# Kernel optimization log

Hardware: AMD Instinct MI355X
Metric: run time of the kernel (lower is better)

The kernel has to match this reference:

```python
import jax, jax.numpy as jnp
import numpy as np

S, B, D, E2 = 2048, 32, 1024, 1024  # src_len, batch, dec_hid_dim, 2*enc_hid_dim


def setup_inputs() -> dict:
    key = jax.random.key(0)
    k1, k2, k3, k4, k5 = jax.random.split(key, 5)
    scale = 1.0 / np.sqrt(D)
    return {
        "dec_prev_hidden": jax.random.normal(k1, (B, D), dtype=jnp.float32),
        "enc_outputs": jax.random.normal(k2, (S, B, E2), dtype=jnp.float32),
        "Wb": jax.random.normal(k3, (D, D), dtype=jnp.float32) * scale,
        "Wc": jax.random.normal(k4, (D, E2), dtype=jnp.float32) * scale,
        "Wa": jax.random.normal(k5, (D,), dtype=jnp.float32) * scale,
    }


def reference(dec_prev_hidden, enc_outputs, Wb, Wc, Wa):
    # weighted_s_t_1: [B, D] broadcast over seq axis; weighted_H: [S, B, D]
    weighted_s = jnp.einsum('bd,ed->be', dec_prev_hidden, Wb)          # [B, D]
    weighted_H = jnp.einsum('sbe,de->sbd', enc_outputs, Wc)            # [S, B, D]
    score = jnp.einsum('sbd,d->sb', jnp.tanh(weighted_H + weighted_s), Wa)  # [S, B]
    # torch F.softmax with no dim on a 3-D tensor -> dim=0 (seq axis)
    attn = jax.nn.softmax(score, axis=0)                               # [S, B]
    # bmm([B,1,S], [B,S,2E]) -> [B,1,2E], then permute -> [1,B,2E]
    context = jnp.einsum('sb,sbe->be', attn, enc_outputs)              # [B, 2E]
    return context[None, :, :]                                         # [1, B, 2E]
```

## Files before the change

kernel.cpp:

```cpp
#include <hip/hip_runtime.h>
#include <hip/hip_bf16.h>
#include <stdint.h>

#define S_LEN 2048
#define BATCH 32
#define MROWS (S_LEN*BATCH)

typedef __attribute__((ext_vector_type(8))) short bf16x8;
typedef __attribute__((ext_vector_type(4))) float f32x4;
typedef unsigned short ushort_t;

__device__ inline unsigned int pk2bf(float a, float b) {
  float2 t; t.x = a; t.y = b;
  __hip_bfloat162 h = __float22bfloat162_rn(t);
  union { __hip_bfloat162 h; unsigned int u; } c; c.h = h;
  return c.u;
}

__device__ inline float bflo(unsigned int u) { return __uint_as_float(u << 16); }
__device__ inline float bfhi(unsigned int u) { return __uint_as_float(u & 0xffff0000u); }

__device__ inline void gload_lds16(const void* g, void* l) {
  __builtin_amdgcn_global_load_lds(
      (const __attribute__((address_space(1))) unsigned int*)g,
      (__attribute__((address_space(3))) unsigned int*)l, 16, 0, 0);
}

__device__ inline float fast_tanh(float x) {
  float e = __expf(2.0f * x);
  return 1.0f - 2.0f / (e + 1.0f);
}

__global__ __launch_bounds__(256) void prep_small_kernel(
    const float* __restrict__ dec, const float* __restrict__ Wb,
    const float* __restrict__ Wc, ushort_t* __restrict__ WcBf,
    float* __restrict__ wsum, float* __restrict__ outZero, int outN)
{
  const int t = threadIdx.x;
  const int bid = blockIdx.x;
  if (bid < 64) {
    const int base = bid * 16384;
    for (int i = 0; i < 16; ++i) {
      int idx = base + i * 1024 + t * 4;
      float4 v = *(const float4*)(Wc + idx);
      uint2 w; w.x = pk2bf(v.x, v.y); w.y = pk2bf(v.z, v.w);
      *(uint2*)(WcBf + idx) = w;
    }
  } else if (bid < 96) {
    const int j = bid - 64;
    __shared__ float sdec[32][65];
    __shared__ float swb[32][65];
    const int b = t & 31, nl = t >> 5;
    float acc0 = 0.f, acc1 = 0.f, acc2 = 0.f, acc3 = 0.f;
    for (int c = 0; c < 16; ++c) {
      __syncthreads();
      for (int idx = t; idx < 2048; idx += 256) {
        int rr = idx >> 6, dd = idx & 63;
        sdec[rr][dd] = dec[rr * 1024 + c * 64 + dd];
        swb[rr][dd]  = Wb[(size_t)(j * 32 + rr) * 1024 + c * 64 + dd];
      }
      __syncthreads();
      #pragma unroll 8
      for (int dd = 0; dd < 64; ++dd) {
        float dv = sdec[b][dd];
        acc0 += dv * swb[nl][dd];
        acc1 += dv * swb[nl + 8][dd];
        acc2 += dv * swb[nl + 16][dd];
        acc3 += dv * swb[nl + 24][dd];
      }
    }
    wsum[b * 1024 + j * 32 + nl]      = acc0;
    wsum[b * 1024 + j * 32 + nl + 8]  = acc1;
    wsum[b * 1024 + j * 32 + nl + 16] = acc2;
    wsum[b * 1024 + j * 32 + nl + 24] = acc3;
  } else {
    float4 z = make_float4(0.f, 0.f, 0.f, 0.f);
    const int n4 = outN >> 2;
    for (int i = t; i < n4; i += 256)
      ((float4*)outZero)[i] = z;
  }
}

__global__ __launch_bounds__(256, 4) void score_kernel(
    const float4* __restrict__ encF4, ushort_t* __restrict__ encBf,
    const ushort_t* __restrict__ WcBf, const float* __restrict__ wsum,
    const float* __restrict__ Wa, float* __restrict__ scoreP8T)
{
  __shared__ ushort_t Ab[128][64];
  __shared__ ushort_t Bb[128][64];
  __shared__ float scorep[128];

  const int tid = threadIdx.x;
  const int lane = tid & 63;
  const int l15 = lane & 15, q = lane >> 4;
  const int r7 = l15 & 7;
  const int wid = tid >> 6;
  const int wr = wid >> 1, wc = wid & 1;
  const int bid = blockIdx.x;
  const int mi = bid & 15, nblk = (bid >> 4) & 7, mg = bid >> 7;
  const size_t rowBase = (size_t)(mg * 16 + mi) * 128;

  if (tid < 128) scorep[tid] = 0.f;

  const int tRow = tid >> 4;
  const int f4 = tid & 15;
  const int swzT = (((f4 >> 1) ^ (tRow & 7)) * 8) + ((f4 & 1) * 4);

  int bOff[4], dOff[4];
  #pragma unroll
  for (int k = 0; k < 4; ++k) {
    const int s = k * 256 + tid;
    const int r = s >> 3, c = s & 7;
    bOff[k] = (int)((nblk * 128 + r) * 1024 + ((c ^ (r & 7)) * 8));
    dOff[k] = s * 8;
  }
  ushort_t* const aL = &Ab[0][0];
  ushort_t* const bL = &Bb[0][0];

  int aRow[4], bRow[4];
  #pragma unroll
  for (int m = 0; m < 4; ++m) aRow[m] = (wr * 64 + m * 16 + l15) * 64;
  #pragma unroll
  for (int n = 0; n < 4; ++n) bRow[n] = (wc * 64 + n * 16 + l15) * 64;
  const int ch0 = (q ^ r7) * 8;
  const int ch1 = ((4 + q) ^ r7) * 8;

  f32x4 acc[4][4];
  #pragma unroll
  for (int m = 0; m < 4; ++m)
    #pragma unroll
    for (int n = 0; n < 4; ++n) { f32x4 z = {0.f,0.f,0.f,0.f}; acc[m][n] = z; }

  for (int kt = 0; kt < 16; ++kt) {
    const int ko = kt * 64;
    #pragma unroll
    for (int k = 0; k < 4; ++k)
      gload_lds16(WcBf + ko + bOff[k], bL + dOff[k]);

    float4 av[8];
    #pragma unroll
    for (int k = 0; k < 8; ++k)
      av[k] = encF4[(rowBase + k * 16 + tRow) * 256 + kt * 16 + f4];

    #pragma unroll
    for (int k = 0; k < 8; ++k) {
      uint2 w;
      w.x = pk2bf(av[k].x, av[k].y);
      w.y = pk2bf(av[k].z, av[k].w);
      const int r = k * 16 + tRow;
      *(uint2*)(aL + r * 64 + swzT) = w;
      if (nblk == 0)
        *(uint2*)(encBf + (rowBase + r) * 1024 + ko + f4 * 4) = w;
    }
    __syncthreads();

    #pragma unroll
    for (int kk = 0; kk < 2; ++kk) {
      const int cho = kk ? ch1 : ch0;
      bf16x8 af[4], bv[4];
      #pragma unroll
      for (int m = 0; m < 4; ++m) af[m] = *(const bf16x8*)(aL + aRow[m] + cho);
      #pragma unroll
      for (int n = 0; n < 4; ++n) bv[n] = *(const bf16x8*)(bL + bRow[n] + cho);
      #pragma unroll
      for (int m = 0; m < 4; ++m)
        #pragma unroll
        for (int n = 0; n < 4; ++n)
          acc[m][n] = __builtin_amdgcn_mfma_f32_16x16x32_bf16(
              af[m], bv[n], acc[m][n], 0, 0, 0);
    }
    __syncthreads();
  }

  #pragma unroll
  for (int m = 0; m < 4; ++m) {
    #pragma unroll
    for (int i = 0; i < 4; ++i) {
      const int rowl = wr * 64 + m * 16 + q * 4 + i;
      const int bb2 = rowl & 31;
      float v = 0.f;
      #pragma unroll
      for (int n = 0; n < 4; ++n) {
        const int col = nblk * 128 + wc * 64 + n * 16 + l15;
        float x = acc[m][n][i] + wsum[bb2 * 1024 + col];
        v += fast_tanh(x) * Wa[col];
      }
      v += __shfl_xor(v, 1); v += __shfl_xor(v, 2);
      v += __shfl_xor(v, 4); v += __shfl_xor(v, 8);
      if (l15 == 0) atomicAdd(&scorep[rowl], v);
    }
  }
  __syncthreads();
  if (tid < 128) {
    const int grow = (int)rowBase + tid;
    const int b = grow & 31, s = grow >> 5;
    scoreP8T[((b * 2048 + s) << 3) + nblk] = scorep[tid];
  }
}

__global__ __launch_bounds__(256) void ctx_kernel(
    const ushort_t* __restrict__ encBf, const float* __restrict__ scoreP8T,
    float* __restrict__ out)
{
  const int b = blockIdx.x & 31, sc = blockIdx.x >> 5;
  const int t = threadIdx.x;
  __shared__ float eCh[64];
  __shared__ float red[256];

  const int chunk0 = sc * 64;
  const float* colBase = scoreP8T + ((size_t)b * 2048 << 3);
  float ssum = 0.f;
  for (int s = t; s < S_LEN; s += 256) {
    const float4* p = (const float4*)(colBase + ((size_t)s << 3));
    float4 u = p[0], v = p[1];
    float scv = ((u.x + u.y) + (u.z + u.w)) + ((v.x + v.y) + (v.z + v.w));
    float e = __expf(scv);
    ssum += e;
    const int d = s - chunk0;
    if ((unsigned)d < 64u) eCh[d] = e;
  }
  red[t] = ssum;
  __syncthreads();
  #pragma unroll
  for (int o = 128; o > 0; o >>= 1) {
    if (t < o) red[t] += red[t + o];
    __syncthreads();
  }
  const float inv = 1.0f / red[0];

  float a0 = 0.f, a1 = 0.f, a2 = 0.f, a3 = 0.f;
  const int e0 = t * 4;
  #pragma unroll 4
  for (int si = 0; si < 64; ++si) {
    const int s = chunk0 + si;
    const float a = eCh[si];
    uint2 w = *(const uint2*)(encBf + ((size_t)s * 32 + b) * 1024 + e0);
    a0 += a * bflo(w.x); a1 += a * bfhi(w.x);
    a2 += a * bflo(w.y); a3 += a * bfhi(w.y);
  }
  float* op = out + b * 1024 + e0;
  atomicAdd(op + 0, a0 * inv); atomicAdd(op + 1, a1 * inv);
  atomicAdd(op + 2, a2 * inv); atomicAdd(op + 3, a3 * inv);
}

extern "C" void kernel_launch(void* const* d_in, const int* in_sizes, int n_in,
                              void* d_out, int out_size, void* d_ws, size_t ws_size,
                              hipStream_t stream) {
  const float* dec = (const float*)d_in[0];
  const float* enc = (const float*)d_in[1];
  const float* Wb  = (const float*)d_in[2];
  const float* Wc  = (const float*)d_in[3];
  const float* Wa  = (const float*)d_in[4];
  float* out = (float*)d_out;
  (void)in_sizes; (void)n_in; (void)ws_size;

  char* ws = (char*)d_ws;
  ushort_t* encBf    = (ushort_t*)ws;
  ushort_t* WcBf     = (ushort_t*)(ws + 134217728);
  float*    wsum     = (float*)(ws + 134217728 + 2097152);
  float*    scoreP8T = (float*)(ws + 134217728 + 2097152 + 131072);

  prep_small_kernel<<<97, 256, 0, stream>>>(dec, Wb, Wc, WcBf, wsum,
                                            out, out_size);
  score_kernel<<<4096, 256, 0, stream>>>((const float4*)enc, encBf, WcBf,
                                         wsum, Wa, scoreP8T);
  ctx_kernel<<<1024, 256, 0, stream>>>(encBf, scoreP8T, out);
}
```

Before: 383.2 us.

## Replace atomic context accumulation with per-chunk partials and a reduce kernel

Each context block previously recomputed the full softmax denominator over all 2048 positions and accumulated into the output with float atomics, which also required zeroing the output beforehand. Now each block computes only its own 64-entry exp sum with a wavefront shuffle and writes partial context vectors to workspace. A new small reduce kernel sums the partials and the per-chunk sums, then normalizes. This removes redundant score reads, the output-zero pass, and atomics, at the cost of an extra launch and 4 MB of partial traffic.

```diff
diff --git a/kernel.cpp b/kernel.cpp
--- a/kernel.cpp
+++ b/kernel.cpp
@@ -34,7 +34,7 @@
 __global__ __launch_bounds__(256) void prep_small_kernel(
     const float* __restrict__ dec, const float* __restrict__ Wb,
     const float* __restrict__ Wc, ushort_t* __restrict__ WcBf,
-    float* __restrict__ wsum, float* __restrict__ outZero, int outN)
+    float* __restrict__ wsum)
 {
   const int t = threadIdx.x;
   const int bid = blockIdx.x;
@@ -46,7 +46,7 @@
       uint2 w; w.x = pk2bf(v.x, v.y); w.y = pk2bf(v.z, v.w);
       *(uint2*)(WcBf + idx) = w;
     }
-  } else if (bid < 96) {
+  } else {
     const int j = bid - 64;
     __shared__ float sdec[32][65];
     __shared__ float swb[32][65];
@@ -73,11 +73,6 @@
     wsum[b * 1024 + j * 32 + nl + 8]  = acc1;
     wsum[b * 1024 + j * 32 + nl + 16] = acc2;
     wsum[b * 1024 + j * 32 + nl + 24] = acc3;
-  } else {
-    float4 z = make_float4(0.f, 0.f, 0.f, 0.f);
-    const int n4 = outN >> 2;
-    for (int i = t; i < n4; i += 256)
-      ((float4*)outZero)[i] = z;
   }
 }
 
@@ -198,35 +193,29 @@
   }
 }
 
-__global__ __launch_bounds__(256) void ctx_kernel(
+__global__ __launch_bounds__(256) void ctx_partial_kernel(
     const ushort_t* __restrict__ encBf, const float* __restrict__ scoreP8T,
-    float* __restrict__ out)
+    float* __restrict__ partial, float* __restrict__ gSum)
 {
   const int b = blockIdx.x & 31, sc = blockIdx.x >> 5;
   const int t = threadIdx.x;
   __shared__ float eCh[64];
-  __shared__ float red[256];
 
   const int chunk0 = sc * 64;
-  const float* colBase = scoreP8T + ((size_t)b * 2048 << 3);
-  float ssum = 0.f;
-  for (int s = t; s < S_LEN; s += 256) {
-    const float4* p = (const float4*)(colBase + ((size_t)s << 3));
+  if (t < 64) {
+    const float4* p = (const float4*)(scoreP8T +
+                        (((size_t)b * 2048 + chunk0 + t) << 3));
     float4 u = p[0], v = p[1];
     float scv = ((u.x + u.y) + (u.z + u.w)) + ((v.x + v.y) + (v.z + v.w));
     float e = __expf(scv);
-    ssum += e;
-    const int d = s - chunk0;
-    if ((unsigned)d < 64u) eCh[d] = e;
-  }
-  red[t] = ssum;
+    eCh[t] = e;
+    float sum = e;
+    sum += __shfl_xor(sum, 1);  sum += __shfl_xor(sum, 2);
+    sum += __shfl_xor(sum, 4);  sum += __shfl_xor(sum, 8);
+    sum += __shfl_xor(sum, 16); sum += __shfl_xor(sum, 32);
+    if (t == 0) gSum[sc * 32 + b] = sum;
+  }
   __syncthreads();
-  #pragma unroll
-  for (int o = 128; o > 0; o >>= 1) {
-    if (t < o) red[t] += red[t + o];
-    __syncthreads();
-  }
-  const float inv = 1.0f / red[0];
 
   float a0 = 0.f, a1 = 0.f, a2 = 0.f, a3 = 0.f;
   const int e0 = t * 4;
@@ -238,9 +227,28 @@
     a0 += a * bflo(w.x); a1 += a * bfhi(w.x);
     a2 += a * bflo(w.y); a3 += a * bfhi(w.y);
   }
-  float* op = out + b * 1024 + e0;
-  atomicAdd(op + 0, a0 * inv); atomicAdd(op + 1, a1 * inv);
-  atomicAdd(op + 2, a2 * inv); atomicAdd(op + 3, a3 * inv);
+  *(float4*)(partial + ((size_t)(sc * 32 + b)) * 1024 + e0) =
+      make_float4(a0, a1, a2, a3);
+}
+
+__global__ __launch_bounds__(256) void ctx_reduce_kernel(
+    const float* __restrict__ partial, const float* __restrict__ gSum,
+    float* __restrict__ out)
+{
+  const int b = blockIdx.x, t = threadIdx.x;
+  float tot = 0.f;
+  #pragma unroll
+  for (int sc = 0; sc < 32; ++sc) tot += gSum[sc * 32 + b];
+  const float inv = 1.0f / tot;
+
+  float4 acc = make_float4(0.f, 0.f, 0.f, 0.f);
+  #pragma unroll
+  for (int sc = 0; sc < 32; ++sc) {
+    float4 v = *(const float4*)(partial + ((size_t)(sc * 32 + b)) * 1024 + t * 4);
+    acc.x += v.x; acc.y += v.y; acc.z += v.z; acc.w += v.w;
+  }
+  acc.x *= inv; acc.y *= inv; acc.z *= inv; acc.w *= inv;
+  *(float4*)(out + (size_t)b * 1024 + t * 4) = acc;
 }
 
 extern "C" void kernel_launch(void* const* d_in, const int* in_sizes, int n_in,
@@ -252,17 +260,19 @@
   const float* Wc  = (const float*)d_in[3];
   const float* Wa  = (const float*)d_in[4];
   float* out = (float*)d_out;
-  (void)in_sizes; (void)n_in; (void)ws_size;
+  (void)in_sizes; (void)n_in; (void)ws_size; (void)out_size;
 
   char* ws = (char*)d_ws;
   ushort_t* encBf    = (ushort_t*)ws;
   ushort_t* WcBf     = (ushort_t*)(ws + 134217728);
   float*    wsum     = (float*)(ws + 134217728 + 2097152);
   float*    scoreP8T = (float*)(ws + 134217728 + 2097152 + 131072);
-
-  prep_small_kernel<<<97, 256, 0, stream>>>(dec, Wb, Wc, WcBf, wsum,
-                                            out, out_size);
+  float*    partial  = (float*)(ws + 134217728 + 2097152 + 131072 + 2097152);
+  float*    gSum     = (float*)(ws + 134217728 + 2097152 + 131072 + 2097152 + 4194304);
+
+  prep_small_kernel<<<96, 256, 0, stream>>>(dec, Wb, Wc, WcBf, wsum);
   score_kernel<<<4096, 256, 0, stream>>>((const float4*)enc, encBf, WcBf,
                                          wsum, Wa, scoreP8T);
-  ctx_kernel<<<1024, 256, 0, stream>>>(encBf, scoreP8T, out);
-}
+  ctx_partial_kernel<<<1024, 256, 0, stream>>>(encBf, scoreP8T, partial, gSum);
+  ctx_reduce_kernel<<<32, 256, 0, stream>>>(partial, gSum, out);
+}
```

After: 367.8 us, median of 2. 1.04x faster.
